# Optimization experiments

Hardware: AMD Instinct MI355X
Metric: run time of the kernel (lower is better)

Reference implementation:

```python
import jax, jax.numpy as jnp
import numpy as np

EMB = 1024

def setup_inputs() -> dict:
    key = jax.random.key(0)
    ks = jax.random.split(key, 7)
    s = 1.0 / np.sqrt(EMB)
    x = jax.random.normal(ks[0], (4, 2048, EMB), dtype=jnp.float32)
    Wk = jax.random.normal(ks[1], (EMB, EMB), dtype=jnp.float32) * s
    bk = jnp.zeros((EMB,), dtype=jnp.float32)
    Wq = jax.random.normal(ks[2], (EMB, EMB), dtype=jnp.float32) * s
    bq = jnp.zeros((EMB,), dtype=jnp.float32)
    Wv = jax.random.normal(ks[3], (EMB, EMB), dtype=jnp.float32) * s
    bv = jnp.zeros((EMB,), dtype=jnp.float32)
    return {"x": x, "Wk": Wk, "bk": bk, "Wq": Wq, "bq": bq, "Wv": Wv, "bv": bv}

def reference(x, Wk, bk, Wq, bq, Wv, bv):
    # Linear layers: x @ W.T + b (torch nn.Linear convention)
    k = jnp.einsum('bse,fe->bsf', x, Wk) + bk
    q = jnp.einsum('bse,fe->bsf', x, Wq) + bq
    v = jnp.einsum('bse,fe->bsf', x, Wv) + bv
    E = x.shape[-1]
    # NOTE: original computes k @ q^T (not q @ k^T) — reproduce faithfully.
    sim = jnp.einsum('bsd,btd->bst', k, q) / jnp.sqrt(jnp.float32(E))
    S = x.shape[1]
    causal = jnp.tril(jnp.ones((S, S), dtype=bool))  # [S,S]
    sim = jnp.where(causal, sim, -jnp.inf)
    attn = jax.nn.softmax(sim, axis=-1)
    return jnp.einsum('bst,btd->bsd', attn, v)
```

## Files before the change

kernel.cpp:

```cpp
#include <hip/hip_runtime.h>
#include <cstdint>


typedef __attribute__((ext_vector_type(8))) _Float16 f16x8;
typedef __attribute__((ext_vector_type(4))) float f32x4;

__device__ __forceinline__ unsigned short f2h(float x) {
  return __builtin_bit_cast(unsigned short, (_Float16)x);
}

__device__ __forceinline__ void lds_dma16(const void* g, void* l) {
  auto gp = reinterpret_cast<const __attribute__((address_space(1))) void*>(
      reinterpret_cast<uintptr_t>(g));
  auto lp = reinterpret_cast<__attribute__((address_space(3))) void*>(
      reinterpret_cast<uintptr_t>(l));
  __builtin_amdgcn_global_load_lds(gp, lp, 16, 0, 0);
}

__device__ __forceinline__ void gemm128(const unsigned short* __restrict__ Ag,
                                        const unsigned short* __restrict__ Bg,
                                        int lda, int ldb, int nk,
                                        unsigned short* As, unsigned short* Bs,
                                        f32x4 acc[4][4]) {
  const int tid = threadIdx.x;
  const int lane = tid & 63, wave = tid >> 6;
  const int wm = wave >> 1, wn = wave & 1;
  const int sr = lane >> 2;
  const int scb = (((lane & 3) ^ ((lane >> 3) & 3)) * 8);
  const int rr = lane & 15, qq = lane >> 4;
  const int slot = ((qq ^ ((rr >> 1) & 3)) * 8);

#pragma unroll
  for (int i = 0; i < 4; ++i)
#pragma unroll
    for (int j = 0; j < 4; ++j) {
      f32x4 z = {0.f, 0.f, 0.f, 0.f};
      acc[i][j] = z;
    }

  const int srow_a = (wave * 2) * 16 + sr;
#pragma unroll
  for (int c = 0; c < 2; ++c) {
    int chunk = wave * 2 + c;
    int row = chunk * 16 + sr;
    lds_dma16(Ag + (size_t)row * lda + scb, As + chunk * 512);
    lds_dma16(Bg + (size_t)row * ldb + scb, Bs + chunk * 512);
  }
  (void)srow_a;

  int buf = 0;
  for (int k0 = 0; k0 < nk; k0 += 32) {
    __syncthreads();
    const int kn = k0 + 32;
    if (kn < nk) {
      unsigned short* An = As + (buf ^ 1) * 4096;
      unsigned short* Bn = Bs + (buf ^ 1) * 4096;
#pragma unroll
      for (int c = 0; c < 2; ++c) {
        int chunk = wave * 2 + c;
        int row = chunk * 16 + sr;
        lds_dma16(Ag + (size_t)row * lda + kn + scb, An + chunk * 512);
        lds_dma16(Bg + (size_t)row * ldb + kn + scb, Bn + chunk * 512);
      }
    }

    f16x8 af[4], bf[4];
    const unsigned short* Ar = As + buf * 4096 + (wm * 64 + rr) * 32 + slot;
    const unsigned short* Br = Bs + buf * 4096 + (wn * 64 + rr) * 32 + slot;
#pragma unroll
    for (int i = 0; i < 4; ++i) af[i] = *(const f16x8*)(Ar + i * 512);
#pragma unroll
    for (int j = 0; j < 4; ++j) bf[j] = *(const f16x8*)(Br + j * 512);
#pragma unroll
    for (int i = 0; i < 4; ++i)
#pragma unroll
      for (int j = 0; j < 4; ++j)
        acc[i][j] = __builtin_amdgcn_mfma_f32_16x16x32_f16(af[i], bf[j],
                                                           acc[i][j], 0, 0, 0);
    buf ^= 1;
  }
}

__global__ void cvt_kernel(const float* __restrict__ x,
                           const float* __restrict__ w0,
                           const float* __restrict__ w1,
                           const float* __restrict__ w2,
                           unsigned short* __restrict__ dst,
                           float* __restrict__ rsum) {
  int i = blockIdx.x * 256 + threadIdx.x;
  if (i >= 2883584) {
    int z2 = i - 2883584;
    float4 z = {0.f, 0.f, 0.f, 0.f};
    ((float4*)rsum)[z2] = z;
    return;
  }
  const float* s;
  size_t si;
  if (i < 2097152) {
    s = x; si = i;
  } else {
    int j = i - 2097152;
    int z = j >> 18;
    s = (z == 0) ? w0 : ((z == 1) ? w1 : w2);
    si = j & 262143;
  }
  float4 f = ((const float4*)s)[si];
  ushort4 u;
  u.x = f2h(f.x); u.y = f2h(f.y); u.z = f2h(f.z); u.w = f2h(f.w);
  ((ushort4*)dst)[i] = u;
}

__global__ __launch_bounds__(256) void qkv_gemm_kernel(
    const unsigned short* __restrict__ xh, const unsigned short* __restrict__ wh,
    const float* __restrict__ bk, const float* __restrict__ bq,
    const float* __restrict__ bv, unsigned short* __restrict__ kh,
    unsigned short* __restrict__ qh, unsigned short* __restrict__ vh) {
  __shared__ unsigned short As[2 * 128 * 32], Bs[2 * 128 * 32];
  const int tn = blockIdx.x & 7, z = blockIdx.x >> 3;
  const unsigned short* W = wh + (size_t)z * 1048576;
  const float* bias = (z == 0) ? bk : ((z == 1) ? bq : bv);
  unsigned short* dst = (z == 0) ? kh : ((z == 1) ? qh : vh);
  const int tm = blockIdx.y;

  f32x4 acc[4][4];
  gemm128(xh + (size_t)tm * 128 * 1024, W + (size_t)tn * 128 * 1024,
          1024, 1024, 1024, As, Bs, acc);

  const int lane = threadIdx.x & 63, wave = threadIdx.x >> 6;
  const int wm = wave >> 1, wn = wave & 1, rr = lane & 15, qq = lane >> 4;
  float bj[4];
#pragma unroll
  for (int j = 0; j < 4; ++j)
    bj[j] = bias[tn * 128 + wn * 64 + j * 16 + rr];
#pragma unroll
  for (int i = 0; i < 4; ++i)
#pragma unroll
    for (int reg = 0; reg < 4; ++reg) {
      int gm = tm * 128 + wm * 64 + i * 16 + qq * 4 + reg;
#pragma unroll
      for (int j = 0; j < 4; ++j) {
        int gc = tn * 128 + wn * 64 + j * 16 + rr;
        dst[(size_t)gm * 1024 + gc] = f2h(acc[i][j][reg] + bj[j]);
      }
    }
}

__global__ __launch_bounds__(256) void transpose_v_kernel(
    const unsigned short* __restrict__ v, unsigned short* __restrict__ vT) {
  __shared__ unsigned short tile[64][65];
  const int b = blockIdx.z;
  const unsigned short* vp = v + (size_t)b * 2048 * 1024;
  unsigned short* vtp = vT + (size_t)b * 1024 * 2048;
  const int t0 = blockIdx.x * 64, d0 = blockIdx.y * 64;
  const int lr = threadIdx.x >> 4, lc = (threadIdx.x & 15) * 4;
#pragma unroll
  for (int p = 0; p < 4; ++p) {
    int tr = p * 16 + lr;
    ushort4 u = *(const ushort4*)(vp + (size_t)(t0 + tr) * 1024 + d0 + lc);
    tile[tr][lc] = u.x; tile[tr][lc + 1] = u.y;
    tile[tr][lc + 2] = u.z; tile[tr][lc + 3] = u.w;
  }
  __syncthreads();
#pragma unroll
  for (int p = 0; p < 4; ++p) {
    int dr = p * 16 + lr;
    ushort4 u;
    u.x = tile[lc][dr]; u.y = tile[lc + 1][dr];
    u.z = tile[lc + 2][dr]; u.w = tile[lc + 3][dr];
    *(ushort4*)(vtp + (size_t)(d0 + dr) * 2048 + t0 + lc) = u;
  }
}

__global__ __launch_bounds__(256) void scores_kernel(
    const unsigned short* __restrict__ kh, const unsigned short* __restrict__ qh,
    unsigned short* __restrict__ P, float* __restrict__ rsum) {
  const int b = blockIdx.y;
  int idx = blockIdx.x;
  int ts = (int)((sqrtf(8.0f * idx + 1.0f) - 1.0f) * 0.5f);
  while ((ts + 1) * (ts + 2) / 2 <= idx) ++ts;
  while (ts * (ts + 1) / 2 > idx) --ts;
  const int tt = idx - ts * (ts + 1) / 2;
  __shared__ unsigned short As[2 * 128 * 32], Bs[2 * 128 * 32];

  f32x4 acc[4][4];
  gemm128(kh + ((size_t)(b * 2048 + ts * 128)) * 1024,
          qh + ((size_t)(b * 2048 + tt * 128)) * 1024,
          1024, 1024, 1024, As, Bs, acc);

  const int lane = threadIdx.x & 63, wave = threadIdx.x >> 6;
  const int wm = wave >> 1, wn = wave & 1, rr = lane & 15, qq = lane >> 4;
  unsigned short* Pb = P + (size_t)b * 2048 * 2048;
  float* rs = rsum + b * 2048;
#pragma unroll
  for (int i = 0; i < 4; ++i)
#pragma unroll
    for (int reg = 0; reg < 4; ++reg) {
      int srow = ts * 128 + wm * 64 + i * 16 + qq * 4 + reg;
      float p = 0.f;
#pragma unroll
      for (int j = 0; j < 4; ++j) {
        int tcol = tt * 128 + wn * 64 + j * 16 + rr;
        float e = (tcol <= srow) ? __expf(acc[i][j][reg] * 0.03125f - 4.0f)
                                 : 0.0f;
        Pb[(size_t)srow * 2048 + tcol] = f2h(e);
        p += e;
      }
#pragma unroll
      for (int off = 1; off < 16; off <<= 1) p += __shfl_xor(p, off);
      if (rr == 0) atomicAdd(rs + srow, p);
    }
}

__global__ __launch_bounds__(256) void pv_gemm_kernel(
    const unsigned short* __restrict__ P, const unsigned short* __restrict__ vT,
    const float* __restrict__ rsum, float* __restrict__ out) {
  const int td = blockIdx.x, ts = 15 - blockIdx.y, b = blockIdx.z;
  __shared__ unsigned short As[2 * 128 * 32], Bs[2 * 128 * 32];

  f32x4 acc[4][4];
  gemm128(P + ((size_t)(b * 2048 + ts * 128)) * 2048,
          vT + ((size_t)(b * 1024 + td * 128)) * 2048,
          2048, 2048, (ts + 1) * 128, As, Bs, acc);

  const int lane = threadIdx.x & 63, wave = threadIdx.x >> 6;
  const int wm = wave >> 1, wn = wave & 1, rr = lane & 15, qq = lane >> 4;
#pragma unroll
  for (int i = 0; i < 4; ++i)
#pragma unroll
    for (int reg = 0; reg < 4; ++reg) {
      int srow = ts * 128 + wm * 64 + i * 16 + qq * 4 + reg;
      float rv = __builtin_amdgcn_rcpf(rsum[b * 2048 + srow]);
#pragma unroll
      for (int j = 0; j < 4; ++j) {
        int dcol = td * 128 + wn * 64 + j * 16 + rr;
        out[((size_t)(b * 2048 + srow)) * 1024 + dcol] = acc[i][j][reg] * rv;
      }
    }
}

extern "C" void kernel_launch(void* const* d_in, const int* in_sizes, int n_in,
                              void* d_out, int out_size, void* d_ws,
                              size_t ws_size, hipStream_t stream) {
  const float* x  = (const float*)d_in[0];
  const float* Wk = (const float*)d_in[1];
  const float* bk = (const float*)d_in[2];
  const float* Wq = (const float*)d_in[3];
  const float* bq = (const float*)d_in[4];
  const float* Wv = (const float*)d_in[5];
  const float* bv = (const float*)d_in[6];
  float* out = (float*)d_out;

  char* ws = (char*)d_ws;
  const size_t MB = 1ull << 20;
  unsigned short* xh = (unsigned short*)(ws + 0);
  unsigned short* wh = (unsigned short*)(ws + 16 * MB);
  unsigned short* vh = (unsigned short*)(ws + 22 * MB);
  unsigned short* P  = (unsigned short*)(ws + 0);
  unsigned short* kh = (unsigned short*)(ws + 38 * MB);
  unsigned short* qh = (unsigned short*)(ws + 54 * MB);
  unsigned short* vT = (unsigned short*)(ws + 70 * MB);
  float* rsum = (float*)(ws + 86 * MB);

  cvt_kernel<<<11272, 256, 0, stream>>>(x, Wk, Wq, Wv, xh, rsum);
  qkv_gemm_kernel<<<dim3(24, 64), 256, 0, stream>>>(xh, wh, bk, bq, bv,
                                                    kh, qh, vh);
  transpose_v_kernel<<<dim3(32, 16, 4), 256, 0, stream>>>(vh, vT);
  scores_kernel<<<dim3(136, 4), 256, 0, stream>>>(kh, qh, P, rsum);
  pv_gemm_kernel<<<dim3(8, 16, 4), 256, 0, stream>>>(P, vT, rsum, out);
}
```

Baseline: 250.6 us.

## Fuse V transpose into QKV epilogue and single-buffer attention GEMMs

The QKV GEMM now writes V directly in transposed layout with vectorized stores, which removes the separate transpose kernel and its extra pass over V in memory. The scores and PV kernels switch to a single-buffered LDS GEMM with a sync before and after each k step, and declare a higher minimum occupancy. This halves their shared memory so more blocks can be resident, at the cost of losing the prefetch overlap between loads and MFMA.

```diff
diff --git a/kernel.cpp b/kernel.cpp
--- a/kernel.cpp
+++ b/kernel.cpp
@@ -38,7 +38,6 @@
       acc[i][j] = z;
     }
 
-  const int srow_a = (wave * 2) * 16 + sr;
 #pragma unroll
   for (int c = 0; c < 2; ++c) {
     int chunk = wave * 2 + c;
@@ -46,7 +45,6 @@
     lds_dma16(Ag + (size_t)row * lda + scb, As + chunk * 512);
     lds_dma16(Bg + (size_t)row * ldb + scb, Bs + chunk * 512);
   }
-  (void)srow_a;
 
   int buf = 0;
   for (int k0 = 0; k0 < nk; k0 += 32) {
@@ -78,6 +76,53 @@
         acc[i][j] = __builtin_amdgcn_mfma_f32_16x16x32_f16(af[i], bf[j],
                                                            acc[i][j], 0, 0, 0);
     buf ^= 1;
+  }
+}
+
+__device__ __forceinline__ void gemm128_sb(
+    const unsigned short* __restrict__ Ag, const unsigned short* __restrict__ Bg,
+    int lda, int ldb, int nk, unsigned short* As, unsigned short* Bs,
+    f32x4 acc[4][4]) {
+  const int tid = threadIdx.x;
+  const int lane = tid & 63, wave = tid >> 6;
+  const int wm = wave >> 1, wn = wave & 1;
+  const int sr = lane >> 2;
+  const int scb = (((lane & 3) ^ ((lane >> 3) & 3)) * 8);
+  const int rr = lane & 15, qq = lane >> 4;
+  const int slot = ((qq ^ ((rr >> 1) & 3)) * 8);
+
+#pragma unroll
+  for (int i = 0; i < 4; ++i)
+#pragma unroll
+    for (int j = 0; j < 4; ++j) {
+      f32x4 z = {0.f, 0.f, 0.f, 0.f};
+      acc[i][j] = z;
+    }
+
+  for (int k0 = 0; k0 < nk; k0 += 32) {
+#pragma unroll
+    for (int c = 0; c < 2; ++c) {
+      int chunk = wave * 2 + c;
+      int row = chunk * 16 + sr;
+      lds_dma16(Ag + (size_t)row * lda + k0 + scb, As + chunk * 512);
+      lds_dma16(Bg + (size_t)row * ldb + k0 + scb, Bs + chunk * 512);
+    }
+    __syncthreads();
+
+    f16x8 af[4], bf[4];
+    const unsigned short* Ar = As + (wm * 64 + rr) * 32 + slot;
+    const unsigned short* Br = Bs + (wn * 64 + rr) * 32 + slot;
+#pragma unroll
+    for (int i = 0; i < 4; ++i) af[i] = *(const f16x8*)(Ar + i * 512);
+#pragma unroll
+    for (int j = 0; j < 4; ++j) bf[j] = *(const f16x8*)(Br + j * 512);
+#pragma unroll
+    for (int i = 0; i < 4; ++i)
+#pragma unroll
+      for (int j = 0; j < 4; ++j)
+        acc[i][j] = __builtin_amdgcn_mfma_f32_16x16x32_f16(af[i], bf[j],
+                                                           acc[i][j], 0, 0, 0);
+    __syncthreads();
   }
 }
 
@@ -114,12 +159,11 @@
     const unsigned short* __restrict__ xh, const unsigned short* __restrict__ wh,
     const float* __restrict__ bk, const float* __restrict__ bq,
     const float* __restrict__ bv, unsigned short* __restrict__ kh,
-    unsigned short* __restrict__ qh, unsigned short* __restrict__ vh) {
+    unsigned short* __restrict__ qh, unsigned short* __restrict__ vT) {
   __shared__ unsigned short As[2 * 128 * 32], Bs[2 * 128 * 32];
   const int tn = blockIdx.x & 7, z = blockIdx.x >> 3;
   const unsigned short* W = wh + (size_t)z * 1048576;
   const float* bias = (z == 0) ? bk : ((z == 1) ? bq : bv);
-  unsigned short* dst = (z == 0) ? kh : ((z == 1) ? qh : vh);
   const int tm = blockIdx.y;
 
   f32x4 acc[4][4];
@@ -132,46 +176,40 @@
 #pragma unroll
   for (int j = 0; j < 4; ++j)
     bj[j] = bias[tn * 128 + wn * 64 + j * 16 + rr];
-#pragma unroll
-  for (int i = 0; i < 4; ++i)
-#pragma unroll
-    for (int reg = 0; reg < 4; ++reg) {
-      int gm = tm * 128 + wm * 64 + i * 16 + qq * 4 + reg;
+
+  if (z == 2) {
+#pragma unroll
+    for (int i = 0; i < 4; ++i) {
+      int gm0 = tm * 128 + wm * 64 + i * 16 + qq * 4;
+      int bb = gm0 >> 11, t0 = gm0 & 2047;
 #pragma unroll
       for (int j = 0; j < 4; ++j) {
         int gc = tn * 128 + wn * 64 + j * 16 + rr;
-        dst[(size_t)gm * 1024 + gc] = f2h(acc[i][j][reg] + bj[j]);
-      }
-    }
-}
-
-__global__ __launch_bounds__(256) void transpose_v_kernel(
-    const unsigned short* __restrict__ v, unsigned short* __restrict__ vT) {
-  __shared__ unsigned short tile[64][65];
-  const int b = blockIdx.z;
-  const unsigned short* vp = v + (size_t)b * 2048 * 1024;
-  unsigned short* vtp = vT + (size_t)b * 1024 * 2048;
-  const int t0 = blockIdx.x * 64, d0 = blockIdx.y * 64;
-  const int lr = threadIdx.x >> 4, lc = (threadIdx.x & 15) * 4;
-#pragma unroll
-  for (int p = 0; p < 4; ++p) {
-    int tr = p * 16 + lr;
-    ushort4 u = *(const ushort4*)(vp + (size_t)(t0 + tr) * 1024 + d0 + lc);
-    tile[tr][lc] = u.x; tile[tr][lc + 1] = u.y;
-    tile[tr][lc + 2] = u.z; tile[tr][lc + 3] = u.w;
-  }
-  __syncthreads();
-#pragma unroll
-  for (int p = 0; p < 4; ++p) {
-    int dr = p * 16 + lr;
-    ushort4 u;
-    u.x = tile[lc][dr]; u.y = tile[lc + 1][dr];
-    u.z = tile[lc + 2][dr]; u.w = tile[lc + 3][dr];
-    *(ushort4*)(vtp + (size_t)(d0 + dr) * 2048 + t0 + lc) = u;
-  }
-}
-
-__global__ __launch_bounds__(256) void scores_kernel(
+        ushort4 u;
+        u.x = f2h(acc[i][j][0] + bj[j]);
+        u.y = f2h(acc[i][j][1] + bj[j]);
+        u.z = f2h(acc[i][j][2] + bj[j]);
+        u.w = f2h(acc[i][j][3] + bj[j]);
+        *(ushort4*)(vT + ((size_t)(bb * 1024 + gc)) * 2048 + t0) = u;
+      }
+    }
+  } else {
+    unsigned short* dst = (z == 0) ? kh : qh;
+#pragma unroll
+    for (int i = 0; i < 4; ++i)
+#pragma unroll
+      for (int reg = 0; reg < 4; ++reg) {
+        int gm = tm * 128 + wm * 64 + i * 16 + qq * 4 + reg;
+#pragma unroll
+        for (int j = 0; j < 4; ++j) {
+          int gc = tn * 128 + wn * 64 + j * 16 + rr;
+          dst[(size_t)gm * 1024 + gc] = f2h(acc[i][j][reg] + bj[j]);
+        }
+      }
+  }
+}
+
+__global__ __launch_bounds__(256, 4) void scores_kernel(
     const unsigned short* __restrict__ kh, const unsigned short* __restrict__ qh,
     unsigned short* __restrict__ P, float* __restrict__ rsum) {
   const int b = blockIdx.y;
@@ -180,12 +218,12 @@
   while ((ts + 1) * (ts + 2) / 2 <= idx) ++ts;
   while (ts * (ts + 1) / 2 > idx) --ts;
   const int tt = idx - ts * (ts + 1) / 2;
-  __shared__ unsigned short As[2 * 128 * 32], Bs[2 * 128 * 32];
+  __shared__ unsigned short As[128 * 32], Bs[128 * 32];
 
   f32x4 acc[4][4];
-  gemm128(kh + ((size_t)(b * 2048 + ts * 128)) * 1024,
-          qh + ((size_t)(b * 2048 + tt * 128)) * 1024,
-          1024, 1024, 1024, As, Bs, acc);
+  gemm128_sb(kh + ((size_t)(b * 2048 + ts * 128)) * 1024,
+             qh + ((size_t)(b * 2048 + tt * 128)) * 1024,
+             1024, 1024, 1024, As, Bs, acc);
 
   const int lane = threadIdx.x & 63, wave = threadIdx.x >> 6;
   const int wm = wave >> 1, wn = wave & 1, rr = lane & 15, qq = lane >> 4;
@@ -211,16 +249,16 @@
     }
 }
 
-__global__ __launch_bounds__(256) void pv_gemm_kernel(
+__global__ __launch_bounds__(256, 4) void pv_gemm_kernel(
     const unsigned short* __restrict__ P, const unsigned short* __restrict__ vT,
     const float* __restrict__ rsum, float* __restrict__ out) {
   const int td = blockIdx.x, ts = 15 - blockIdx.y, b = blockIdx.z;
-  __shared__ unsigned short As[2 * 128 * 32], Bs[2 * 128 * 32];
+  __shared__ unsigned short As[128 * 32], Bs[128 * 32];
 
   f32x4 acc[4][4];
-  gemm128(P + ((size_t)(b * 2048 + ts * 128)) * 2048,
-          vT + ((size_t)(b * 1024 + td * 128)) * 2048,
-          2048, 2048, (ts + 1) * 128, As, Bs, acc);
+  gemm128_sb(P + ((size_t)(b * 2048 + ts * 128)) * 2048,
+             vT + ((size_t)(b * 1024 + td * 128)) * 2048,
+             2048, 2048, (ts + 1) * 128, As, Bs, acc);
 
   const int lane = threadIdx.x & 63, wave = threadIdx.x >> 6;
   const int wm = wave >> 1, wn = wave & 1, rr = lane & 15, qq = lane >> 4;
@@ -254,7 +292,6 @@
   const size_t MB = 1ull << 20;
   unsigned short* xh = (unsigned short*)(ws + 0);
   unsigned short* wh = (unsigned short*)(ws + 16 * MB);
-  unsigned short* vh = (unsigned short*)(ws + 22 * MB);
   unsigned short* P  = (unsigned short*)(ws + 0);
   unsigned short* kh = (unsigned short*)(ws + 38 * MB);
   unsigned short* qh = (unsigned short*)(ws + 54 * MB);
@@ -263,8 +300,7 @@
 
   cvt_kernel<<<11272, 256, 0, stream>>>(x, Wk, Wq, Wv, xh, rsum);
   qkv_gemm_kernel<<<dim3(24, 64), 256, 0, stream>>>(xh, wh, bk, bq, bv,
-                                                    kh, qh, vh);
-  transpose_v_kernel<<<dim3(32, 16, 4), 256, 0, stream>>>(vh, vT);
+                                                    kh, qh, vT);
   scores_kernel<<<dim3(136, 4), 256, 0, stream>>>(kh, qh, P, rsum);
   pv_gemm_kernel<<<dim3(8, 16, 4), 256, 0, stream>>>(P, vT, rsum, out);
 }
```

Measured after the change: 256.3 us. +2.2%, slower.

## Fuse V transpose into QKV GEMM by computing V^T directly

Applied to the files above, without the earlier changes.

For the V projection, the GEMM operands are swapped so each block computes W·x^T tiles and writes V transposed straight into vT, with the bias added per output row. This removes the separate transpose kernel and the intermediate V buffer round trip through memory. The pv epilogue also loads four row sums at once as a float4 instead of one scalar per row. The transposed stores keep the 16-lane contiguous pattern, so coalescing should be similar to before.

```diff
diff --git a/kernel.cpp b/kernel.cpp
--- a/kernel.cpp
+++ b/kernel.cpp
@@ -38,7 +38,6 @@
       acc[i][j] = z;
     }
 
-  const int srow_a = (wave * 2) * 16 + sr;
 #pragma unroll
   for (int c = 0; c < 2; ++c) {
     int chunk = wave * 2 + c;
@@ -46,7 +45,6 @@
     lds_dma16(Ag + (size_t)row * lda + scb, As + chunk * 512);
     lds_dma16(Bg + (size_t)row * ldb + scb, Bs + chunk * 512);
   }
-  (void)srow_a;
 
   int buf = 0;
   for (int k0 = 0; k0 < nk; k0 += 32) {
@@ -114,60 +112,59 @@
     const unsigned short* __restrict__ xh, const unsigned short* __restrict__ wh,
     const float* __restrict__ bk, const float* __restrict__ bq,
     const float* __restrict__ bv, unsigned short* __restrict__ kh,
-    unsigned short* __restrict__ qh, unsigned short* __restrict__ vh) {
+    unsigned short* __restrict__ qh, unsigned short* __restrict__ vT) {
   __shared__ unsigned short As[2 * 128 * 32], Bs[2 * 128 * 32];
   const int tn = blockIdx.x & 7, z = blockIdx.x >> 3;
   const unsigned short* W = wh + (size_t)z * 1048576;
-  const float* bias = (z == 0) ? bk : ((z == 1) ? bq : bv);
-  unsigned short* dst = (z == 0) ? kh : ((z == 1) ? qh : vh);
   const int tm = blockIdx.y;
 
+  const unsigned short* Ag = (z == 2) ? (W + (size_t)tn * 128 * 1024)
+                                      : (xh + (size_t)tm * 128 * 1024);
+  const unsigned short* Bg = (z == 2) ? (xh + (size_t)tm * 128 * 1024)
+                                      : (W + (size_t)tn * 128 * 1024);
+
   f32x4 acc[4][4];
-  gemm128(xh + (size_t)tm * 128 * 1024, W + (size_t)tn * 128 * 1024,
-          1024, 1024, 1024, As, Bs, acc);
+  gemm128(Ag, Bg, 1024, 1024, 1024, As, Bs, acc);
 
   const int lane = threadIdx.x & 63, wave = threadIdx.x >> 6;
   const int wm = wave >> 1, wn = wave & 1, rr = lane & 15, qq = lane >> 4;
-  float bj[4];
-#pragma unroll
-  for (int j = 0; j < 4; ++j)
-    bj[j] = bias[tn * 128 + wn * 64 + j * 16 + rr];
-#pragma unroll
-  for (int i = 0; i < 4; ++i)
-#pragma unroll
-    for (int reg = 0; reg < 4; ++reg) {
-      int gm = tm * 128 + wm * 64 + i * 16 + qq * 4 + reg;
-#pragma unroll
-      for (int j = 0; j < 4; ++j) {
-        int gc = tn * 128 + wn * 64 + j * 16 + rr;
-        dst[(size_t)gm * 1024 + gc] = f2h(acc[i][j][reg] + bj[j]);
-      }
-    }
-}
-
-__global__ __launch_bounds__(256) void transpose_v_kernel(
-    const unsigned short* __restrict__ v, unsigned short* __restrict__ vT) {
-  __shared__ unsigned short tile[64][65];
-  const int b = blockIdx.z;
-  const unsigned short* vp = v + (size_t)b * 2048 * 1024;
-  unsigned short* vtp = vT + (size_t)b * 1024 * 2048;
-  const int t0 = blockIdx.x * 64, d0 = blockIdx.y * 64;
-  const int lr = threadIdx.x >> 4, lc = (threadIdx.x & 15) * 4;
-#pragma unroll
-  for (int p = 0; p < 4; ++p) {
-    int tr = p * 16 + lr;
-    ushort4 u = *(const ushort4*)(vp + (size_t)(t0 + tr) * 1024 + d0 + lc);
-    tile[tr][lc] = u.x; tile[tr][lc + 1] = u.y;
-    tile[tr][lc + 2] = u.z; tile[tr][lc + 3] = u.w;
-  }
-  __syncthreads();
-#pragma unroll
-  for (int p = 0; p < 4; ++p) {
-    int dr = p * 16 + lr;
-    ushort4 u;
-    u.x = tile[lc][dr]; u.y = tile[lc + 1][dr];
-    u.z = tile[lc + 2][dr]; u.w = tile[lc + 3][dr];
-    *(ushort4*)(vtp + (size_t)(d0 + dr) * 2048 + t0 + lc) = u;
+
+  if (z == 2) {
+#pragma unroll
+    for (int i = 0; i < 4; ++i) {
+      int d0 = tn * 128 + wm * 64 + i * 16 + qq * 4;
+      float4 bi = *(const float4*)(bv + d0);
+      float bir[4] = {bi.x, bi.y, bi.z, bi.w};
+#pragma unroll
+      for (int reg = 0; reg < 4; ++reg) {
+        int d = d0 + reg;
+#pragma unroll
+        for (int j = 0; j < 4; ++j) {
+          int tg = tm * 128 + wn * 64 + j * 16 + rr;
+          int bb = tg >> 11, tt = tg & 2047;
+          vT[((size_t)(bb * 1024 + d)) * 2048 + tt] =
+              f2h(acc[i][j][reg] + bir[reg]);
+        }
+      }
+    }
+  } else {
+    const float* bias = (z == 0) ? bk : bq;
+    unsigned short* dst = (z == 0) ? kh : qh;
+    float bj[4];
+#pragma unroll
+    for (int j = 0; j < 4; ++j)
+      bj[j] = bias[tn * 128 + wn * 64 + j * 16 + rr];
+#pragma unroll
+    for (int i = 0; i < 4; ++i)
+#pragma unroll
+      for (int reg = 0; reg < 4; ++reg) {
+        int gm = tm * 128 + wm * 64 + i * 16 + qq * 4 + reg;
+#pragma unroll
+        for (int j = 0; j < 4; ++j) {
+          int gc = tn * 128 + wn * 64 + j * 16 + rr;
+          dst[(size_t)gm * 1024 + gc] = f2h(acc[i][j][reg] + bj[j]);
+        }
+      }
   }
 }
 
@@ -225,17 +222,22 @@
   const int lane = threadIdx.x & 63, wave = threadIdx.x >> 6;
   const int wm = wave >> 1, wn = wave & 1, rr = lane & 15, qq = lane >> 4;
 #pragma unroll
-  for (int i = 0; i < 4; ++i)
+  for (int i = 0; i < 4; ++i) {
+    int s0 = ts * 128 + wm * 64 + i * 16 + qq * 4;
+    float4 r4 = *(const float4*)(rsum + b * 2048 + s0);
+    float rv[4] = {__builtin_amdgcn_rcpf(r4.x), __builtin_amdgcn_rcpf(r4.y),
+                   __builtin_amdgcn_rcpf(r4.z), __builtin_amdgcn_rcpf(r4.w)};
 #pragma unroll
     for (int reg = 0; reg < 4; ++reg) {
-      int srow = ts * 128 + wm * 64 + i * 16 + qq * 4 + reg;
-      float rv = __builtin_amdgcn_rcpf(rsum[b * 2048 + srow]);
+      int srow = s0 + reg;
 #pragma unroll
       for (int j = 0; j < 4; ++j) {
         int dcol = td * 128 + wn * 64 + j * 16 + rr;
-        out[((size_t)(b * 2048 + srow)) * 1024 + dcol] = acc[i][j][reg] * rv;
-      }
-    }
+        out[((size_t)(b * 2048 + srow)) * 1024 + dcol] =
+            acc[i][j][reg] * rv[reg];
+      }
+    }
+  }
 }
 
 extern "C" void kernel_launch(void* const* d_in, const int* in_sizes, int n_in,
@@ -254,7 +256,6 @@
   const size_t MB = 1ull << 20;
   unsigned short* xh = (unsigned short*)(ws + 0);
   unsigned short* wh = (unsigned short*)(ws + 16 * MB);
-  unsigned short* vh = (unsigned short*)(ws + 22 * MB);
   unsigned short* P  = (unsigned short*)(ws + 0);
   unsigned short* kh = (unsigned short*)(ws + 38 * MB);
   unsigned short* qh = (unsigned short*)(ws + 54 * MB);
@@ -263,8 +264,7 @@
 
   cvt_kernel<<<11272, 256, 0, stream>>>(x, Wk, Wq, Wv, xh, rsum);
   qkv_gemm_kernel<<<dim3(24, 64), 256, 0, stream>>>(xh, wh, bk, bq, bv,
-                                                    kh, qh, vh);
-  transpose_v_kernel<<<dim3(32, 16, 4), 256, 0, stream>>>(vh, vT);
+                                                    kh, qh, vT);
   scores_kernel<<<dim3(136, 4), 256, 0, stream>>>(kh, qh, P, rsum);
   pv_gemm_kernel<<<dim3(8, 16, 4), 256, 0, stream>>>(P, vT, rsum, out);
 }
```

Result: no change. 245.8 us (-1.9%).
